# Kernel optimization log

Hardware: AMD Instinct MI355X
Metric: run time of the kernel (lower is better)

The kernel has to match this reference:

```python
import jax, jax.numpy as jnp
import numpy as np

N = 100000
E = 1600000
D = 128

def setup_inputs() -> dict:
    key = jax.random.key(0)
    ks = jax.random.split(key, 8)
    s = 1.0 / np.sqrt(D)
    x = jax.random.normal(ks[0], (N, D), dtype=jnp.float32)
    Wl1 = jax.random.uniform(ks[1], (D, D), jnp.float32, -s, s)
    bl1 = jnp.zeros((D,), jnp.float32)
    Wr1 = jax.random.uniform(ks[2], (D, D), jnp.float32, -s, s)
    Wl2 = jax.random.uniform(ks[3], (D, D), jnp.float32, -s, s)
    bl2 = jnp.zeros((D,), jnp.float32)
    Wr2 = jax.random.uniform(ks[4], (D, D), jnp.float32, -s, s)
    edge_index = jax.random.randint(ks[5], (2, E), 0, N, dtype=jnp.int64)
    return {"x": x, "Wl1": Wl1, "bl1": bl1, "Wr1": Wr1,
            "Wl2": Wl2, "bl2": bl2, "Wr2": Wr2, "edge_index": edge_index}

def _sage_layer(x, src, dst, Wl, bl, Wr, num_nodes):
    # mean aggregation of source features onto destination nodes
    msg = x[src]                                               # [E, D] gather
    ssum = jax.ops.segment_sum(msg, dst, num_segments=num_nodes)
    deg = jax.ops.segment_sum(jnp.ones((src.shape[0], 1), x.dtype), dst,
                              num_segments=num_nodes)
    agg = ssum / jnp.maximum(deg, 1.0)
    # out = lin_l(agg) + lin_r(x); lin_l has bias, lin_r has none (PyG SAGEConv)
    return agg @ Wl + bl + x @ Wr

def reference(x, Wl1, bl1, Wr1, Wl2, bl2, Wr2, edge_index):
    src, dst = edge_index[0], edge_index[1]
    n = x.shape[0]
    h = jax.nn.relu(_sage_layer(x, src, dst, Wl1, bl1, Wr1, n))
    # dropout is identity at inference
    h = jax.nn.relu(_sage_layer(h, src, dst, Wl2, bl2, Wr2, n))
    return h
```

## Files before the change

kernel.cpp:

```cpp
#include <hip/hip_runtime.h>
#include <cstdint>

typedef float f4 __attribute__((ext_vector_type(4)));
typedef float f2 __attribute__((ext_vector_type(2)));
typedef short bfv8 __attribute__((ext_vector_type(8)));

__device__ inline f4 f4_zero(){ f4 v = {0.f,0.f,0.f,0.f}; return v; }

__device__ inline uint32_t f2bf(float f){
    uint32_t u = __float_as_uint(f);
    return (u + 0x7fffu + ((u >> 16) & 1u)) >> 16;
}
__device__ inline uint32_t pack_bf2(float a, float b){
    return f2bf(a) | (f2bf(b) << 16);
}
__device__ inline f2 bf2_unpack(uint32_t v){
    f2 r;
    r[0] = __uint_as_float(v << 16);
    r[1] = __uint_as_float(v & 0xffff0000u);
    return r;
}

#define PB 64

__global__ __launch_bounds__(256) void k_tobf16(const f4* __restrict__ in,
                                                uint2* __restrict__ out, int n4){
    int i = blockIdx.x * 256 + threadIdx.x;
    if (i >= n4) return;
    f4 v = in[i];
    uint2 o;
    o.x = pack_bf2(v[0], v[1]);
    o.y = pack_bf2(v[2], v[3]);
    out[i] = o;
}

__global__ void k_detect(const uint32_t* __restrict__ p, int* __restrict__ flag){
    __shared__ int nz;
    if (threadIdx.x == 0) nz = 0;
    __syncthreads();
    int local = 0;
    for (int i = threadIdx.x; i < 2048; i += blockDim.x)
        if (p[2*i + 1] != 0u) local = 1;
    if (local) atomicOr(&nz, 1);
    __syncthreads();
    if (threadIdx.x == 0) *flag = (nz == 0) ? 1 : 0;
}

__global__ __launch_bounds__(1024) void k_hist(const void* __restrict__ eidx, int E, int NB,
                                               const int* __restrict__ flag,
                                               int* __restrict__ blkhist){
    __shared__ int lh[1024];
    int t = threadIdx.x, blk = blockIdx.x;
    for (int i = t; i < NB; i += 1024) lh[i] = 0;
    __syncthreads();
    int R = (E + PB - 1) / PB;
    int s = blk * R, e_end = s + R < E ? s + R : E;
    bool is64 = (*flag != 0);
    const uint32_t* p32 = (const uint32_t*)eidx;
    const int*      pi  = (const int*)eidx;
    for (int e = s + t; e < e_end; e += 1024){
        int d = is64 ? (int)p32[2*(size_t)(E + e)] : pi[(size_t)E + e];
        atomicAdd(&lh[d >> 7], 1);
    }
    __syncthreads();
    for (int i = t; i < NB; i += 1024)
        blkhist[(size_t)i * PB + blk] = lh[i];
}

__global__ __launch_bounds__(1024) void k_offsets(const int* __restrict__ blkhist,
                                                  int NB,
                                                  int* __restrict__ coff,
                                                  int* __restrict__ offs){
    __shared__ int tot_s[1024];
    __shared__ int excl_s[1024];
    __shared__ int ws[16];
    int t = threadIdx.x, lane = t & 63, w = t >> 6;
    int v = 0;
    if (t < NB){
        const int4* row = (const int4*)(blkhist + (size_t)t * PB);
        #pragma unroll
        for (int i = 0; i < PB/4; ++i){
            int4 q = row[i];
            v += q.x + q.y + q.z + q.w;
        }
    }
    tot_s[t] = v;
    __syncthreads();
    int x = tot_s[t];
    int vv = x;
    #pragma unroll
    for (int off = 1; off < 64; off <<= 1){
        int u = __shfl_up(x, off, 64);
        if (lane >= off) x += u;
    }
    if (lane == 63) ws[w] = x;
    __syncthreads();
    if (w == 0 && lane < 16){
        int y = ws[lane];
        #pragma unroll
        for (int off = 1; off < 16; off <<= 1){
            int u = __shfl_up(y, off, 64);
            if (lane >= off) y += u;
        }
        ws[lane] = y;
    }
    __syncthreads();
    int incl = x + (w ? ws[w - 1] : 0);
    int excl = incl - vv;
    excl_s[t] = excl;
    if (t < NB)      coff[t] = excl;
    if (t == NB - 1) coff[NB] = incl;
    __syncthreads();
    if (t < NB){
        const int4* row  = (const int4*)(blkhist + (size_t)t * PB);
        int4*       orow = (int4*)(offs + (size_t)t * PB);
        int run = excl_s[t];
        #pragma unroll
        for (int i = 0; i < PB/4; ++i){
            int4 q = row[i];
            int4 o;
            o.x = run; run += q.x;
            o.y = run; run += q.y;
            o.z = run; run += q.z;
            o.w = run; run += q.w;
            orow[i] = o;
        }
    }
}

__global__ __launch_bounds__(1024) void k_scatter(const void* __restrict__ eidx, int E, int NB,
                                                  const int* __restrict__ flag,
                                                  const int* __restrict__ offs,
                                                  uint32_t* __restrict__ bucketed){
    __shared__ int cur[1024];
    int t = threadIdx.x, blk = blockIdx.x;
    for (int i = t; i < NB; i += 1024) cur[i] = offs[(size_t)i * PB + blk];
    __syncthreads();
    int R = (E + PB - 1) / PB;
    int s = blk * R, e_end = s + R < E ? s + R : E;
    bool is64 = (*flag != 0);
    const uint32_t* p32 = (const uint32_t*)eidx;
    const int*      pi  = (const int*)eidx;
    for (int e = s + t; e < e_end; e += 1024){
        int sv, dv;
        if (is64){ sv = (int)p32[2*(size_t)e]; dv = (int)p32[2*(size_t)(E + e)]; }
        else     { sv = pi[e];                 dv = pi[(size_t)E + e]; }
        int b = dv >> 7;
        int pos = atomicAdd(&cur[b], 1);
        bucketed[pos] = ((uint32_t)(dv & 127) << 17) | (uint32_t)sv;
    }
}

__global__ __launch_bounds__(1024) void k_bucketsort(const uint32_t* __restrict__ bucketed,
                                                     const int* __restrict__ coff,
                                                     int* __restrict__ esrc,
                                                     int* __restrict__ rowptr,
                                                     int N, int E, int NB){
    __shared__ int hist[128], cur[128], wtot[2];
    int b = blockIdx.x, t = threadIdx.x;
    if (t < 128) hist[t] = 0;
    __syncthreads();
    int s = coff[b], e_end = coff[b + 1];
    for (int i = s + t; i < e_end; i += 1024)
        atomicAdd(&hist[bucketed[i] >> 17], 1);
    __syncthreads();
    int x = 0, v = 0;
    if (t < 128){
        int lane = t & 63;
        v = hist[t]; x = v;
        #pragma unroll
        for (int off = 1; off < 64; off <<= 1){
            int u = __shfl_up(x, off, 64);
            if (lane >= off) x += u;
        }
        if (lane == 63) wtot[t >> 6] = x;
    }
    __syncthreads();
    if (t < 128){
        int w = t >> 6;
        int excl = x - v + (w ? wtot[0] : 0);
        int abs0 = s + excl;
        cur[t] = abs0;
        int node = b * 128 + t;
        if (node < N) rowptr[node] = abs0;
    }
    if (b == NB - 1 && t == 0) rowptr[N] = E;
    __syncthreads();
    for (int i = s + t; i < e_end; i += 1024){
        uint32_t val = bucketed[i];
        int r = (int)(val >> 17);
        int pos = atomicAdd(&cur[r], 1);
        esrc[pos] = (int)(val & 0x1FFFFu);
    }
}

__global__ __launch_bounds__(256) void k_aggregate(const uint32_t* __restrict__ featb,
                                                   const int* __restrict__ rowptr,
                                                   const int* __restrict__ esrc,
                                                   uint32_t* __restrict__ aggb, int N){
    int node = blockIdx.x * 4 + (threadIdx.x >> 6);
    if (node >= N) return;
    int lane = threadIdx.x & 63;
    int half = lane >> 5;
    int l8   = lane & 31;
    int b = rowptr[node], e = rowptr[node + 1];
    f2 c0lo={0.f,0.f}, c0hi={0.f,0.f}, c1lo={0.f,0.f}, c1hi={0.f,0.f};
    f2 c2lo={0.f,0.f}, c2hi={0.f,0.f}, c3lo={0.f,0.f}, c3hi={0.f,0.f};
    for (int base = b; base < e; base += 64){
        int m = e - base; if (m > 64) m = 64;
        int idx = (lane < m) ? esrc[base + lane] : 0;
        int j = 0;
        for (; j + 8 <= m; j += 8){
            int s0 = __shfl(idx, j     + half, 64);
            int s1 = __shfl(idx, j + 2 + half, 64);
            int s2 = __shfl(idx, j + 4 + half, 64);
            int s3 = __shfl(idx, j + 6 + half, 64);
            uint2 g0 = *(const uint2*)(featb + (size_t)s0 * 64 + l8 * 2);
            uint2 g1 = *(const uint2*)(featb + (size_t)s1 * 64 + l8 * 2);
            uint2 g2 = *(const uint2*)(featb + (size_t)s2 * 64 + l8 * 2);
            uint2 g3 = *(const uint2*)(featb + (size_t)s3 * 64 + l8 * 2);
            c0lo += bf2_unpack(g0.x); c0hi += bf2_unpack(g0.y);
            c1lo += bf2_unpack(g1.x); c1hi += bf2_unpack(g1.y);
            c2lo += bf2_unpack(g2.x); c2hi += bf2_unpack(g2.y);
            c3lo += bf2_unpack(g3.x); c3hi += bf2_unpack(g3.y);
        }
        for (; j < m; j += 2){
            int jj = j + half;
            int s0 = __shfl(idx, jj < m ? jj : j, 64);
            uint2 g = *(const uint2*)(featb + (size_t)s0 * 64 + l8 * 2);
            if (jj < m){ c0lo += bf2_unpack(g.x); c0hi += bf2_unpack(g.y); }
        }
    }
    f2 lo = (c0lo + c1lo) + (c2lo + c3lo);
    f2 hi = (c0hi + c1hi) + (c2hi + c3hi);
    lo[0] += __shfl_xor(lo[0], 32, 64);
    lo[1] += __shfl_xor(lo[1], 32, 64);
    hi[0] += __shfl_xor(hi[0], 32, 64);
    hi[1] += __shfl_xor(hi[1], 32, 64);
    if (half == 0){
        int deg = e - b;
        float scl = 1.0f / (float)(deg > 1 ? deg : 1);
        uint2 o;
        o.x = pack_bf2(lo[0] * scl, lo[1] * scl);
        o.y = pack_bf2(hi[0] * scl, hi[1] * scl);
        *(uint2*)(aggb + (size_t)node * 64 + l8 * 2) = o;
    }
}

__global__ __launch_bounds__(256) void k_wprep(const float* __restrict__ Wl,
                                               const float* __restrict__ Wr,
                                               uint32_t* __restrict__ Bsw){
    int t = blockIdx.x * 256 + threadIdx.x;
    int s = t >> 9, ct = (t >> 6) & 7, l = t & 63;
    int k0 = s * 32 + (l >> 4) * 8;
    int c  = ct * 16 + (l & 15);
    unsigned short e[8];
    #pragma unroll
    for (int j = 0; j < 8; ++j){
        int k = k0 + j;
        float v = (k < 128) ? Wl[(size_t)k * 128 + c] : Wr[(size_t)(k - 128) * 128 + c];
        e[j] = (unsigned short)f2bf(v);
    }
    uint32_t* o = Bsw + (size_t)t * 4;
    o[0] = (uint32_t)e[0] | ((uint32_t)e[1] << 16);
    o[1] = (uint32_t)e[2] | ((uint32_t)e[3] << 16);
    o[2] = (uint32_t)e[4] | ((uint32_t)e[5] << 16);
    o[3] = (uint32_t)e[6] | ((uint32_t)e[7] << 16);
}

__global__ __launch_bounds__(256) void k_sage_mfma(
    const uint32_t* __restrict__ A1b, const uint32_t* __restrict__ A2b,
    const uint32_t* __restrict__ Bsw, const float* __restrict__ bias,
    float* __restrict__ outf, uint32_t* __restrict__ outbf, int M)
{
    int tid = threadIdx.x;
    int w = tid >> 6, l = tid & 63;
    int l15 = l & 15, l4 = l >> 4;
    int row = blockIdx.x * 64 + w * 16 + l15;
    int rowc = row < M ? row : M - 1;
    const char* a1p = (const char*)(A1b + (size_t)rowc * 64) + l4 * 16;
    const char* a2p = (const char*)(A2b + (size_t)rowc * 64) + l4 * 16;
    const char* bp  = (const char*)Bsw + (size_t)l * 16;

    f4 acc[8];
    #pragma unroll
    for (int ct = 0; ct < 8; ++ct) acc[ct] = f4_zero();

    #pragma unroll
    for (int s = 0; s < 8; ++s){
        bfv8 a = *(const bfv8*)((s < 4 ? a1p : a2p) + (s & 3) * 64);
        #pragma unroll
        for (int ct = 0; ct < 8; ++ct){
            bfv8 b = *(const bfv8*)(bp + (size_t)(s * 8 + ct) * 1024);
            acc[ct] = __builtin_amdgcn_mfma_f32_16x16x32_bf16(a, b, acc[ct], 0, 0, 0);
        }
    }

    int orow0 = blockIdx.x * 64 + w * 16 + l4 * 4;
    #pragma unroll
    for (int ct = 0; ct < 8; ++ct){
        int col = ct * 16 + l15;
        float bb = bias[col];
        #pragma unroll
        for (int r = 0; r < 4; ++r){
            int orow = orow0 + r;
            if (orow < M){
                float v = acc[ct][r] + bb;
                v = v > 0.f ? v : 0.f;
                if (outf)  outf[(size_t)orow * 128 + col] = v;
                if (outbf) ((unsigned short*)outbf)[(size_t)orow * 128 + col] =
                               (unsigned short)f2bf(v);
            }
        }
    }
}

extern "C" void kernel_launch(void* const* d_in, const int* in_sizes, int n_in,
                              void* d_out, int out_size, void* d_ws, size_t ws_size,
                              hipStream_t stream) {
    const float* x    = (const float*)d_in[0];
    const float* Wl1  = (const float*)d_in[1];
    const float* bl1  = (const float*)d_in[2];
    const float* Wr1  = (const float*)d_in[3];
    const float* Wl2  = (const float*)d_in[4];
    const float* bl2  = (const float*)d_in[5];
    const float* Wr2  = (const float*)d_in[6];
    const void*  eidx = d_in[7];
    float* out = (float*)d_out;

    const int N  = in_sizes[0] / 128;
    const int E  = in_sizes[7] / 2;
    const int NB = (N + 127) >> 7;

    char* ws = (char*)d_ws;
    size_t off = 0;
    auto alloc = [&](size_t bytes) -> void* {
        void* p = ws + off;
        off += (bytes + 255) & ~(size_t)255;
        return p;
    };
    int*      flag     = (int*)     alloc(4);
    int*      blkhist  = (int*)     alloc((size_t)NB * PB * 4);
    int*      coff     = (int*)     alloc((size_t)(NB + 1) * 4);
    int*      offs     = (int*)     alloc((size_t)NB * PB * 4);
    int*      esrc     = (int*)     alloc((size_t)E * 4);
    int*      rowptr   = (int*)     alloc((size_t)(N + 1) * 4);
    uint32_t* bsw1     = (uint32_t*)alloc(65536);
    uint32_t* bsw2     = (uint32_t*)alloc(65536);
    size_t uA = (size_t)E * 4 > (size_t)N * 256 ? (size_t)E * 4 : (size_t)N * 256;
    uint32_t* unionA   = (uint32_t*)alloc(uA);
    uint32_t* bucketed = unionA;
    uint32_t* aggb     = unionA;
    uint32_t* unionB   = (uint32_t*)alloc((size_t)N * 256);
    uint32_t* xbf      = unionB;
    uint32_t* hbf      = unionB;

    const int GB = (N + 63) / 64;

    k_tobf16    <<<(N * 32 + 255) / 256, 256, 0, stream>>>((const f4*)x, (uint2*)xbf, N * 32);
    k_wprep     <<<16, 256, 0, stream>>>(Wl1, Wr1, bsw1);
    k_wprep     <<<16, 256, 0, stream>>>(Wl2, Wr2, bsw2);
    k_detect    <<<1, 256, 0, stream>>>((const uint32_t*)eidx, flag);
    k_hist      <<<PB, 1024, 0, stream>>>(eidx, E, NB, flag, blkhist);
    k_offsets   <<<1, 1024, 0, stream>>>(blkhist, NB, coff, offs);
    k_scatter   <<<PB, 1024, 0, stream>>>(eidx, E, NB, flag, offs, bucketed);
    k_bucketsort<<<NB, 1024, 0, stream>>>(bucketed, coff, esrc, rowptr, N, E, NB);

    k_aggregate<<<(N + 3) / 4, 256, 0, stream>>>(xbf, rowptr, esrc, aggb, N);
    k_sage_mfma<<<GB, 256, 0, stream>>>(aggb, xbf, bsw1, bl1, nullptr, hbf, N);

    k_aggregate<<<(N + 3) / 4, 256, 0, stream>>>(hbf, rowptr, esrc, aggb, N);
    k_sage_mfma<<<GB, 256, 0, stream>>>(aggb, hbf, bsw2, bl2, out, nullptr, N);
}
```

Before: 393.8 us.

## Widen edge-sort grid, inline index-width detection, deepen aggregate gather unroll

The histogram and scatter grids grow from 64 to 256 blocks so the edge-sorting passes use more of the GPU. The separate single-block dtype detection kernel is dropped, and each block now redoes the check itself, which saves a launch at the cost of redundant reads. The aggregation loop now issues eight independent feature gathers per step with eight accumulator pairs instead of four, to keep more memory requests in flight. This raises register pressure and makes the prefix-offset kernel scan a larger per-bucket row.

```diff
diff --git a/kernel.cpp b/kernel.cpp
--- a/kernel.cpp
+++ b/kernel.cpp
@@ -6,6 +6,7 @@
 typedef short bfv8 __attribute__((ext_vector_type(8)));
 
 __device__ inline f4 f4_zero(){ f4 v = {0.f,0.f,0.f,0.f}; return v; }
+__device__ inline f2 f2_zero(){ f2 v = {0.f,0.f}; return v; }
 
 __device__ inline uint32_t f2bf(float f){
     uint32_t u = __float_as_uint(f);
@@ -21,7 +22,19 @@
     return r;
 }
 
-#define PB 64
+#define PB 256
+
+__device__ inline bool detect_is64(const uint32_t* p, int* sflag){
+    int t = threadIdx.x;
+    if (t == 0) *sflag = 0;
+    __syncthreads();
+    int local = 0;
+    for (int i = t; i < 2048; i += blockDim.x)
+        if (p[2*i + 1] != 0u) local = 1;
+    if (local) atomicOr(sflag, 1);
+    __syncthreads();
+    return *sflag == 0;
+}
 
 __global__ __launch_bounds__(256) void k_tobf16(const f4* __restrict__ in,
                                                 uint2* __restrict__ out, int n4){
@@ -34,28 +47,16 @@
     out[i] = o;
 }
 
-__global__ void k_detect(const uint32_t* __restrict__ p, int* __restrict__ flag){
-    __shared__ int nz;
-    if (threadIdx.x == 0) nz = 0;
-    __syncthreads();
-    int local = 0;
-    for (int i = threadIdx.x; i < 2048; i += blockDim.x)
-        if (p[2*i + 1] != 0u) local = 1;
-    if (local) atomicOr(&nz, 1);
-    __syncthreads();
-    if (threadIdx.x == 0) *flag = (nz == 0) ? 1 : 0;
-}
-
 __global__ __launch_bounds__(1024) void k_hist(const void* __restrict__ eidx, int E, int NB,
-                                               const int* __restrict__ flag,
                                                int* __restrict__ blkhist){
     __shared__ int lh[1024];
+    __shared__ int dflag;
+    bool is64 = detect_is64((const uint32_t*)eidx, &dflag);
     int t = threadIdx.x, blk = blockIdx.x;
     for (int i = t; i < NB; i += 1024) lh[i] = 0;
     __syncthreads();
     int R = (E + PB - 1) / PB;
     int s = blk * R, e_end = s + R < E ? s + R : E;
-    bool is64 = (*flag != 0);
     const uint32_t* p32 = (const uint32_t*)eidx;
     const int*      pi  = (const int*)eidx;
     for (int e = s + t; e < e_end; e += 1024){
@@ -78,7 +79,7 @@
     int v = 0;
     if (t < NB){
         const int4* row = (const int4*)(blkhist + (size_t)t * PB);
-        #pragma unroll
+        #pragma unroll 8
         for (int i = 0; i < PB/4; ++i){
             int4 q = row[i];
             v += q.x + q.y + q.z + q.w;
@@ -115,7 +116,7 @@
         const int4* row  = (const int4*)(blkhist + (size_t)t * PB);
         int4*       orow = (int4*)(offs + (size_t)t * PB);
         int run = excl_s[t];
-        #pragma unroll
+        #pragma unroll 8
         for (int i = 0; i < PB/4; ++i){
             int4 q = row[i];
             int4 o;
@@ -129,16 +130,16 @@
 }
 
 __global__ __launch_bounds__(1024) void k_scatter(const void* __restrict__ eidx, int E, int NB,
-                                                  const int* __restrict__ flag,
                                                   const int* __restrict__ offs,
                                                   uint32_t* __restrict__ bucketed){
     __shared__ int cur[1024];
+    __shared__ int dflag;
+    bool is64 = detect_is64((const uint32_t*)eidx, &dflag);
     int t = threadIdx.x, blk = blockIdx.x;
     for (int i = t; i < NB; i += 1024) cur[i] = offs[(size_t)i * PB + blk];
     __syncthreads();
     int R = (E + PB - 1) / PB;
     int s = blk * R, e_end = s + R < E ? s + R : E;
-    bool is64 = (*flag != 0);
     const uint32_t* p32 = (const uint32_t*)eidx;
     const int*      pi  = (const int*)eidx;
     for (int e = s + t; e < e_end; e += 1024){
@@ -204,13 +205,41 @@
     int half = lane >> 5;
     int l8   = lane & 31;
     int b = rowptr[node], e = rowptr[node + 1];
-    f2 c0lo={0.f,0.f}, c0hi={0.f,0.f}, c1lo={0.f,0.f}, c1hi={0.f,0.f};
-    f2 c2lo={0.f,0.f}, c2hi={0.f,0.f}, c3lo={0.f,0.f}, c3hi={0.f,0.f};
+    f2 lo0=f2_zero(),lo1=f2_zero(),lo2=f2_zero(),lo3=f2_zero();
+    f2 lo4=f2_zero(),lo5=f2_zero(),lo6=f2_zero(),lo7=f2_zero();
+    f2 hi0=f2_zero(),hi1=f2_zero(),hi2=f2_zero(),hi3=f2_zero();
+    f2 hi4=f2_zero(),hi5=f2_zero(),hi6=f2_zero(),hi7=f2_zero();
     for (int base = b; base < e; base += 64){
         int m = e - base; if (m > 64) m = 64;
         int idx = (lane < m) ? esrc[base + lane] : 0;
         int j = 0;
-        for (; j + 8 <= m; j += 8){
+        for (; j + 16 <= m; j += 16){
+            int s0 = __shfl(idx, j      + half, 64);
+            int s1 = __shfl(idx, j + 2  + half, 64);
+            int s2 = __shfl(idx, j + 4  + half, 64);
+            int s3 = __shfl(idx, j + 6  + half, 64);
+            int s4 = __shfl(idx, j + 8  + half, 64);
+            int s5 = __shfl(idx, j + 10 + half, 64);
+            int s6 = __shfl(idx, j + 12 + half, 64);
+            int s7 = __shfl(idx, j + 14 + half, 64);
+            uint2 g0 = *(const uint2*)(featb + (size_t)s0 * 64 + l8 * 2);
+            uint2 g1 = *(const uint2*)(featb + (size_t)s1 * 64 + l8 * 2);
+            uint2 g2 = *(const uint2*)(featb + (size_t)s2 * 64 + l8 * 2);
+            uint2 g3 = *(const uint2*)(featb + (size_t)s3 * 64 + l8 * 2);
+            uint2 g4 = *(const uint2*)(featb + (size_t)s4 * 64 + l8 * 2);
+            uint2 g5 = *(const uint2*)(featb + (size_t)s5 * 64 + l8 * 2);
+            uint2 g6 = *(const uint2*)(featb + (size_t)s6 * 64 + l8 * 2);
+            uint2 g7 = *(const uint2*)(featb + (size_t)s7 * 64 + l8 * 2);
+            lo0 += bf2_unpack(g0.x); hi0 += bf2_unpack(g0.y);
+            lo1 += bf2_unpack(g1.x); hi1 += bf2_unpack(g1.y);
+            lo2 += bf2_unpack(g2.x); hi2 += bf2_unpack(g2.y);
+            lo3 += bf2_unpack(g3.x); hi3 += bf2_unpack(g3.y);
+            lo4 += bf2_unpack(g4.x); hi4 += bf2_unpack(g4.y);
+            lo5 += bf2_unpack(g5.x); hi5 += bf2_unpack(g5.y);
+            lo6 += bf2_unpack(g6.x); hi6 += bf2_unpack(g6.y);
+            lo7 += bf2_unpack(g7.x); hi7 += bf2_unpack(g7.y);
+        }
+        if (j + 8 <= m){
             int s0 = __shfl(idx, j     + half, 64);
             int s1 = __shfl(idx, j + 2 + half, 64);
             int s2 = __shfl(idx, j + 4 + half, 64);
@@ -219,20 +248,21 @@
             uint2 g1 = *(const uint2*)(featb + (size_t)s1 * 64 + l8 * 2);
             uint2 g2 = *(const uint2*)(featb + (size_t)s2 * 64 + l8 * 2);
             uint2 g3 = *(const uint2*)(featb + (size_t)s3 * 64 + l8 * 2);
-            c0lo += bf2_unpack(g0.x); c0hi += bf2_unpack(g0.y);
-            c1lo += bf2_unpack(g1.x); c1hi += bf2_unpack(g1.y);
-            c2lo += bf2_unpack(g2.x); c2hi += bf2_unpack(g2.y);
-            c3lo += bf2_unpack(g3.x); c3hi += bf2_unpack(g3.y);
+            lo0 += bf2_unpack(g0.x); hi0 += bf2_unpack(g0.y);
+            lo1 += bf2_unpack(g1.x); hi1 += bf2_unpack(g1.y);
+            lo2 += bf2_unpack(g2.x); hi2 += bf2_unpack(g2.y);
+            lo3 += bf2_unpack(g3.x); hi3 += bf2_unpack(g3.y);
+            j += 8;
         }
         for (; j < m; j += 2){
             int jj = j + half;
             int s0 = __shfl(idx, jj < m ? jj : j, 64);
             uint2 g = *(const uint2*)(featb + (size_t)s0 * 64 + l8 * 2);
-            if (jj < m){ c0lo += bf2_unpack(g.x); c0hi += bf2_unpack(g.y); }
-        }
-    }
-    f2 lo = (c0lo + c1lo) + (c2lo + c3lo);
-    f2 hi = (c0hi + c1hi) + (c2hi + c3hi);
+            if (jj < m){ lo0 += bf2_unpack(g.x); hi0 += bf2_unpack(g.y); }
+        }
+    }
+    f2 lo = ((lo0 + lo1) + (lo2 + lo3)) + ((lo4 + lo5) + (lo6 + lo7));
+    f2 hi = ((hi0 + hi1) + (hi2 + hi3)) + ((hi4 + hi5) + (hi6 + hi7));
     lo[0] += __shfl_xor(lo[0], 32, 64);
     lo[1] += __shfl_xor(lo[1], 32, 64);
     hi[0] += __shfl_xor(hi[0], 32, 64);
@@ -339,7 +369,6 @@
         off += (bytes + 255) & ~(size_t)255;
         return p;
     };
-    int*      flag     = (int*)     alloc(4);
     int*      blkhist  = (int*)     alloc((size_t)NB * PB * 4);
     int*      coff     = (int*)     alloc((size_t)(NB + 1) * 4);
     int*      offs     = (int*)     alloc((size_t)NB * PB * 4);
@@ -360,10 +389,9 @@
     k_tobf16    <<<(N * 32 + 255) / 256, 256, 0, stream>>>((const f4*)x, (uint2*)xbf, N * 32);
     k_wprep     <<<16, 256, 0, stream>>>(Wl1, Wr1, bsw1);
     k_wprep     <<<16, 256, 0, stream>>>(Wl2, Wr2, bsw2);
-    k_detect    <<<1, 256, 0, stream>>>((const uint32_t*)eidx, flag);
-    k_hist      <<<PB, 1024, 0, stream>>>(eidx, E, NB, flag, blkhist);
+    k_hist      <<<PB, 1024, 0, stream>>>(eidx, E, NB, blkhist);
     k_offsets   <<<1, 1024, 0, stream>>>(blkhist, NB, coff, offs);
-    k_scatter   <<<PB, 1024, 0, stream>>>(eidx, E, NB, flag, offs, bucketed);
+    k_scatter   <<<PB, 1024, 0, stream>>>(eidx, E, NB, offs, bucketed);
     k_bucketsort<<<NB, 1024, 0, stream>>>(bucketed, coff, esrc, rowptr, N, E, NB);
 
     k_aggregate<<<(N + 3) / 4, 256, 0, stream>>>(xbf, rowptr, esrc, aggb, N);
```

Result: slower. 422.8 us (+7.4%).
